# Kernel optimization log

Hardware: AMD Instinct MI355X
Metric: run time of the kernel (lower is better)

## Reference

```python
import jax, jax.numpy as jnp
import numpy as np

# ---- column/activation layout (matches transformer_info init kwarg) ----
N_COLS = 20          # continuous data columns
MODES = 50           # VGM modes per column (gumbel-softmax width)
SPAN = MODES + 1     # 1 tanh scalar + MODES gumbel logits
IN_DIM = 2048
OUT_DIM = N_COLS * SPAN  # 1020
TAU = 0.2
B = 16384
EPS = 1e-9

_spans = []
for i in range(N_COLS):
    st = i * SPAN
    _spans.append((st, st + 1, 0))          # tanh span (alpha)
    _spans.append((st + 1, st + SPAN, 1))   # gumbel-softmax span (beta/d)
N_SEG = len(_spans)

_seg = np.zeros(OUT_DIM, np.int32)   # segment id per output feature
_typ = np.zeros(OUT_DIM, np.int32)   # 0 = tanh, 1 = gumbel-softmax
for si, (s, e, t) in enumerate(_spans):
    _seg[s:e] = si
    _typ[s:e] = t
SEG = jnp.asarray(_seg)
TYP = jnp.asarray(_typ)


def setup_inputs() -> dict:
    key = jax.random.key(0)
    kx, kw, kb, ku = jax.random.split(key, 4)
    bound = 1.0 / np.sqrt(IN_DIM)  # init_bounded(dim=input_dim)
    x = jax.random.normal(kx, (B, IN_DIM), dtype=jnp.float32)
    W = jax.random.uniform(kw, (IN_DIM, OUT_DIM), minval=-bound, maxval=bound, dtype=jnp.float32)
    b = jax.random.uniform(kb, (OUT_DIM,), minval=-bound, maxval=bound, dtype=jnp.float32)
    u = jax.random.uniform(ku, (B, OUT_DIM), dtype=jnp.float32)  # uniform driving gumbel noise
    return {"x": x, "W": W, "b": b, "u": u}


def _segment_softmax(z):
    # softmax over each transformer_info span, fused via segment ops.
    zT = z.T  # [D, B]
    m = jax.ops.segment_max(zT, SEG, num_segments=N_SEG)      # [S, B]
    e = jnp.exp(zT - m[SEG])
    s = jax.ops.segment_sum(e, SEG, num_segments=N_SEG)       # [S, B]
    return (e / s[SEG]).T  # [B, D]


def reference(x, W, b, u):
    outputs = x @ W + b  # [B, OUT_DIM]
    # Gumbel(0,1) noise from uniform u
    g = -jnp.log(-jnp.log(jnp.clip(u, EPS, 1.0 - EPS)))
    soft = _segment_softmax((outputs + g) / TAU)
    # type 0 -> tanh, type 1 -> gumbel-softmax (single fused select)
    data_t = jnp.where(TYP == 0, jnp.tanh(outputs), soft)
    return outputs, data_t
```

## Files before the change

kernel.cpp:

```cpp
#include <hip/hip_runtime.h>
#include <stdint.h>

#define MDIM 16384
#define NDIM 1020
#define KDIM 2048
#define NPAD 1024

typedef __attribute__((ext_vector_type(4))) float f32x4;
typedef __attribute__((ext_vector_type(8))) short short8;

__device__ __forceinline__ unsigned short f2bf(float f) {
    unsigned int u = __float_as_uint(f);
    unsigned int r = (u + 0x7FFFu + ((u >> 16) & 1u)) >> 16;
    return (unsigned short)r;
}

__global__ void prep_w_kernel(const float* __restrict__ W,
                              unsigned short* __restrict__ Wt) {
    const int id = blockIdx.x * 256 + threadIdx.x;
    const int n0 = (id & 255) * 4;
    const int k0 = (id >> 8) * 4;
    float a[4][4];
    if (n0 < NDIM) {
#pragma unroll
        for (int i = 0; i < 4; ++i) {
            const float* p = W + (size_t)(k0 + i) * NDIM + n0;
            a[i][0] = p[0]; a[i][1] = p[1]; a[i][2] = p[2]; a[i][3] = p[3];
        }
    } else {
#pragma unroll
        for (int i = 0; i < 4; ++i)
#pragma unroll
            for (int j = 0; j < 4; ++j) a[i][j] = 0.f;
    }
#pragma unroll
    for (int j = 0; j < 4; ++j) {
        uint2 p;
        p.x = (unsigned)f2bf(a[0][j]) | ((unsigned)f2bf(a[1][j]) << 16);
        p.y = (unsigned)f2bf(a[2][j]) | ((unsigned)f2bf(a[3][j]) << 16);
        *(uint2*)(Wt + (size_t)(n0 + j) * KDIM + k0) = p;
    }
}

__global__ void prep_x_kernel(const float* __restrict__ x,
                              unsigned short* __restrict__ Xb) {
    const size_t total = (size_t)MDIM * KDIM;
    const size_t stride = (size_t)gridDim.x * 256 * 8;
    for (size_t i = ((size_t)blockIdx.x * 256 + threadIdx.x) * 8; i < total; i += stride) {
        const float4 v0 = *(const float4*)(x + i);
        const float4 v1 = *(const float4*)(x + i + 4);
        uint4 p;
        p.x = (unsigned)f2bf(v0.x) | ((unsigned)f2bf(v0.y) << 16);
        p.y = (unsigned)f2bf(v0.z) | ((unsigned)f2bf(v0.w) << 16);
        p.z = (unsigned)f2bf(v1.x) | ((unsigned)f2bf(v1.y) << 16);
        p.w = (unsigned)f2bf(v1.z) | ((unsigned)f2bf(v1.w) << 16);
        *(uint4*)(Xb + i) = p;
    }
}

__global__ void gemm_bf_kernel(const unsigned short* __restrict__ Xb,
                               const unsigned short* __restrict__ Wt,
                               const float* __restrict__ bias,
                               float* __restrict__ out) {
    __shared__ __align__(16) unsigned short As[128][32];
    __shared__ __align__(16) unsigned short Bs[128][32];

    const int tid  = threadIdx.x;
    const int lane = tid & 63;
    const int wid  = tid >> 6;
    const int wr   = wid >> 1;
    const int wc   = wid & 1;
    const int bn   = blockIdx.x;
    const int bm   = blockIdx.y;

    f32x4 acc[4][4];
#pragma unroll
    for (int i = 0; i < 4; ++i)
#pragma unroll
        for (int j = 0; j < 4; ++j) {
            f32x4 z = {0.f, 0.f, 0.f, 0.f};
            acc[i][j] = z;
        }

    const unsigned short* abase =
        Xb + (size_t)(bm * 128 + wid * 16 + (lane >> 2)) * KDIM + (lane & 3) * 8;
    const unsigned short* bbase =
        Wt + (size_t)(bn * 128 + wid * 16 + (lane >> 2)) * KDIM + (lane & 3) * 8;

    for (int kt = 0; kt < KDIM; kt += 32) {
#pragma unroll
        for (int j = 0; j < 2; ++j) {
            __builtin_amdgcn_global_load_lds(
                (const __attribute__((address_space(1))) unsigned int*)(abase + (size_t)j * 64 * KDIM + kt),
                (__attribute__((address_space(3))) unsigned int*)(&As[j * 64 + wid * 16][0]),
                16, 0, 0);
        }
#pragma unroll
        for (int j = 0; j < 2; ++j) {
            __builtin_amdgcn_global_load_lds(
                (const __attribute__((address_space(1))) unsigned int*)(bbase + (size_t)j * 64 * KDIM + kt),
                (__attribute__((address_space(3))) unsigned int*)(&Bs[j * 64 + wid * 16][0]),
                16, 0, 0);
        }
        __syncthreads();

        short8 af[4], bfr[4];
#pragma unroll
        for (int mi = 0; mi < 4; ++mi)
            af[mi] = *(const short8*)&As[wr * 64 + mi * 16 + (lane & 15)][(lane >> 4) * 8];
#pragma unroll
        for (int ni = 0; ni < 4; ++ni)
            bfr[ni] = *(const short8*)&Bs[wc * 64 + ni * 16 + (lane & 15)][(lane >> 4) * 8];

#pragma unroll
        for (int mi = 0; mi < 4; ++mi)
#pragma unroll
            for (int ni = 0; ni < 4; ++ni)
                acc[mi][ni] = __builtin_amdgcn_mfma_f32_16x16x32_bf16(
                    af[mi], bfr[ni], acc[mi][ni], 0, 0, 0);

        __syncthreads();
    }

#pragma unroll
    for (int ni = 0; ni < 4; ++ni) {
        const int col = bn * 128 + wc * 64 + ni * 16 + (lane & 15);
        if (col < NDIM) {
            const float bv = bias[col];
#pragma unroll
            for (int mi = 0; mi < 4; ++mi) {
                const int row = bm * 128 + wr * 64 + mi * 16 + ((lane >> 4) << 2);
                float* op = out + (size_t)row * NDIM + col;
#pragma unroll
                for (int r = 0; r < 4; ++r)
                    op[(size_t)r * NDIM] = acc[mi][ni][r] + bv;
            }
        }
    }
}

__global__ void gemm_kernel(const float* __restrict__ x,
                            const unsigned short* __restrict__ Wt,
                            const float* __restrict__ bias,
                            float* __restrict__ out) {
    __shared__ __align__(16) unsigned short As[128][32];
    __shared__ __align__(16) unsigned short Bs[128][32];

    const int tid  = threadIdx.x;
    const int lane = tid & 63;
    const int wid  = tid >> 6;
    const int wr   = wid >> 1;
    const int wc   = wid & 1;
    const int bn   = blockIdx.x;
    const int bm   = blockIdx.y;

    f32x4 acc[4][4];
#pragma unroll
    for (int i = 0; i < 4; ++i)
#pragma unroll
        for (int j = 0; j < 4; ++j) {
            f32x4 z = {0.f, 0.f, 0.f, 0.f};
            acc[i][j] = z;
        }

    const int arow = tid >> 3;
    const int akg  = tid & 7;
    const float* xbase = x + (size_t)(bm * 128) * KDIM + akg * 4;
    const unsigned short* wbase =
        Wt + (size_t)(bn * 128 + wid * 32 + (lane >> 2)) * KDIM + (lane & 3) * 8;

    for (int kt = 0; kt < KDIM; kt += 32) {
#pragma unroll
        for (int i = 0; i < 4; ++i) {
            const float4 v = *(const float4*)(xbase + (size_t)(i * 32 + arow) * KDIM + kt);
            uint2 p;
            p.x = (unsigned)f2bf(v.x) | ((unsigned)f2bf(v.y) << 16);
            p.y = (unsigned)f2bf(v.z) | ((unsigned)f2bf(v.w) << 16);
            *(uint2*)&As[i * 32 + arow][akg * 4] = p;
        }
#pragma unroll
        for (int j = 0; j < 2; ++j) {
            const unsigned short* src = wbase + (size_t)j * 16 * KDIM + kt;
            __builtin_amdgcn_global_load_lds(
                (const __attribute__((address_space(1))) unsigned int*)src,
                (__attribute__((address_space(3))) unsigned int*)(&Bs[wid * 32 + j * 16][0]),
                16, 0, 0);
        }
        __syncthreads();

        short8 af[4], bfr[4];
#pragma unroll
        for (int mi = 0; mi < 4; ++mi)
            af[mi] = *(const short8*)&As[wr * 64 + mi * 16 + (lane & 15)][(lane >> 4) * 8];
#pragma unroll
        for (int ni = 0; ni < 4; ++ni)
            bfr[ni] = *(const short8*)&Bs[wc * 64 + ni * 16 + (lane & 15)][(lane >> 4) * 8];

#pragma unroll
        for (int mi = 0; mi < 4; ++mi)
#pragma unroll
            for (int ni = 0; ni < 4; ++ni)
                acc[mi][ni] = __builtin_amdgcn_mfma_f32_16x16x32_bf16(
                    af[mi], bfr[ni], acc[mi][ni], 0, 0, 0);

        __syncthreads();
    }

#pragma unroll
    for (int ni = 0; ni < 4; ++ni) {
        const int col = bn * 128 + wc * 64 + ni * 16 + (lane & 15);
        if (col < NDIM) {
            const float bv = bias[col];
#pragma unroll
            for (int mi = 0; mi < 4; ++mi) {
                const int row = bm * 128 + wr * 64 + mi * 16 + ((lane >> 4) << 2);
                float* op = out + (size_t)row * NDIM + col;
#pragma unroll
                for (int r = 0; r < 4; ++r)
                    op[(size_t)r * NDIM] = acc[mi][ni][r] + bv;
            }
        }
    }
}

__global__ void act_kernel(const float* __restrict__ outp,
                           const float* __restrict__ u,
                           float* __restrict__ dt) {
    const int lane  = threadIdx.x & 63;
    const int gwave = (blockIdx.x * 256 + threadIdx.x) >> 6;
    const int nwave = gridDim.x * 4;
    const int total = MDIM * 20;
    const float NEG_INF = -__builtin_inff();

    for (int unit = gwave; unit < total; unit += nwave) {
        const int row = unit / 20;
        const int sp  = unit - row * 20;
        const size_t base = (size_t)row * NDIM + sp * 51;

        float o = 0.f, uu = 0.5f;
        if (lane < 51) {
            o  = outp[base + lane];
            uu = u[base + lane];
        }
        const bool soft = (lane >= 1) && (lane < 51);

        const float uc = fmaxf(uu, 1e-9f);
        const float g  = -__logf(-__logf(uc));
        float z = soft ? (o + g) * 5.0f : NEG_INF;

        float m = z;
#pragma unroll
        for (int off = 32; off; off >>= 1) m = fmaxf(m, __shfl_xor(m, off));
        float e = soft ? __expf(z - m) : 0.f;
        float s = e;
#pragma unroll
        for (int off = 32; off; off >>= 1) s += __shfl_xor(s, off);

        float res;
        if (lane == 0) {
            const float ex = __expf(-2.0f * fabsf(o));
            const float t  = (1.0f - ex) / (1.0f + ex);
            res = copysignf(t, o);
        } else {
            res = e / s;
        }
        if (lane < 51) dt[base + lane] = res;
    }
}

extern "C" void kernel_launch(void* const* d_in, const int* in_sizes, int n_in,
                              void* d_out, int out_size, void* d_ws, size_t ws_size,
                              hipStream_t stream) {
    const float* x = (const float*)d_in[0];
    const float* W = (const float*)d_in[1];
    const float* b = (const float*)d_in[2];
    const float* u = (const float*)d_in[3];
    float* out = (float*)d_out;
    float* dt  = out + (size_t)MDIM * NDIM;
    unsigned short* Wt = (unsigned short*)d_ws;

    prep_w_kernel<<<512, 256, 0, stream>>>(W, Wt);

    const size_t need = ((size_t)NPAD * KDIM + (size_t)MDIM * KDIM) * sizeof(unsigned short);
    if (ws_size >= need) {
        unsigned short* Xb = Wt + (size_t)NPAD * KDIM;
        prep_x_kernel<<<2048, 256, 0, stream>>>(x, Xb);
        gemm_bf_kernel<<<dim3(8, 128), 256, 0, stream>>>(Xb, Wt, b, out);
    } else {
        gemm_kernel<<<dim3(8, 128), 256, 0, stream>>>(x, Wt, b, out);
    }

    act_kernel<<<8192, 256, 0, stream>>>(out, u, dt);
}
```

Before: 212.3 us.

## Add 256x256-tile double-buffered bf16 GEMM with swizzled LDS and staged prefetch

Adds a new GEMM kernel using 256x256 output tiles, 8 waves and 128KB of dynamic LDS. It double-buffers K-steps of 64, interleaving global_load_lds prefetches with MFMA phases under explicit vmcnt waits, barriers and setprio. It also applies an XOR swizzle to LDS columns to avoid bank conflicts and remaps block ids for L2 locality. The larger tiles cut global traffic and sync overhead per FLOP, but 256 blocks on the GPU is coarse-grained, LDS use is very high, and the ws-size guard and fp32 fallback path are removed.

```diff
diff --git a/kernel.cpp b/kernel.cpp
--- a/kernel.cpp
+++ b/kernel.cpp
@@ -5,9 +5,12 @@
 #define NDIM 1020
 #define KDIM 2048
 #define NPAD 1024
+#define TK   (KDIM / 64)
 
 typedef __attribute__((ext_vector_type(4))) float f32x4;
 typedef __attribute__((ext_vector_type(8))) short short8;
+
+#define MFMA16(a, b, c) __builtin_amdgcn_mfma_f32_16x16x32_bf16((a), (b), (c), 0, 0, 0)
 
 __device__ __forceinline__ unsigned short f2bf(float f) {
     unsigned int u = __float_as_uint(f);
@@ -58,6 +61,183 @@
     }
 }
 
+extern "C" __global__ __launch_bounds__(512, 2) void gemm8_kernel(
+    const unsigned short* __restrict__ Xb,
+    const unsigned short* __restrict__ Wt,
+    const float* __restrict__ bias,
+    float* __restrict__ out) {
+    extern __shared__ unsigned short lds_raw[];
+
+    const int tid  = threadIdx.x;
+    const int lane = tid & 63;
+    const int wid  = tid >> 6;
+    const int wr   = wid >> 2;
+    const int wc   = wid & 3;
+
+    const int bid = blockIdx.x;
+    const int swz = (bid & 7) * 32 + (bid >> 3);
+    const int bm  = swz >> 2;
+    const int bn  = swz & 3;
+
+    const int srow = wid * 8 + (lane >> 3);
+    const int scb  = ((lane & 7) ^ (lane >> 3)) * 8;
+    const unsigned short* aS = Xb + (size_t)(bm * 256 + srow) * KDIM + scb;
+    const unsigned short* bS = Wt + (size_t)(bn * 256 + srow) * KDIM + scb;
+
+#define LDS_A(B) (lds_raw + (B) * 32768)
+#define LDS_B(B) (lds_raw + (B) * 32768 + 16384)
+
+#define STAGE(BUFI, OP, STRIPE, S) do {                                          \
+    const size_t ks_ = (size_t)(((S) * 64) & (KDIM - 1));                        \
+    const unsigned short* sp_ =                                                  \
+        ((OP) ? bS : aS) + (size_t)((STRIPE) * 64) * KDIM + ks_;                 \
+    __builtin_amdgcn_global_load_lds(                                            \
+        (const __attribute__((address_space(1))) unsigned int*)sp_,              \
+        (__attribute__((address_space(3))) unsigned int*)(lds_raw +              \
+            (BUFI) * 32768 + (OP) * 16384 + ((STRIPE) * 64 + wid * 8) * 64),     \
+        16, 0, 0);                                                               \
+} while (0)
+
+#define LOAD_AF(DST, BUFI, MF) do {                                              \
+    _Pragma("unroll")                                                            \
+    for (int k2_ = 0; k2_ < 2; ++k2_) {                                          \
+        const int cb_ = ((k2_ * 4 + (lane >> 4)) ^ (lane & 7)) * 8;              \
+        DST[k2_] = *(const short8*)(LDS_A(BUFI) +                                \
+            (wr * 128 + (MF) * 16 + (lane & 15)) * 64 + cb_);                    \
+    }                                                                            \
+} while (0)
+
+#define VMCNT4 do {                                                              \
+    asm volatile("s_waitcnt vmcnt(4)" ::: "memory");                             \
+    __builtin_amdgcn_sched_barrier(0);                                           \
+} while (0)
+
+    f32x4 acc[8][4];
+#pragma unroll
+    for (int i = 0; i < 8; ++i)
+#pragma unroll
+        for (int j = 0; j < 4; ++j) {
+            f32x4 z = {0.f, 0.f, 0.f, 0.f};
+            acc[i][j] = z;
+        }
+
+    STAGE(0, 0, 0, 0); STAGE(0, 0, 1, 0); STAGE(0, 0, 2, 0); STAGE(0, 0, 3, 0);
+    STAGE(0, 1, 0, 0); STAGE(0, 1, 1, 0); STAGE(0, 1, 2, 0); STAGE(0, 1, 3, 0);
+    STAGE(1, 1, 0, 1); STAGE(1, 1, 1, 1); STAGE(1, 1, 2, 1); STAGE(1, 1, 3, 1);
+    STAGE(1, 0, 0, 1); STAGE(1, 0, 2, 1);
+    VMCNT4;
+    __builtin_amdgcn_s_barrier();
+
+    for (int t = 0; t < TK; ++t) {
+        const int buf = t & 1;
+        const int nb  = buf ^ 1;
+        short8 bfv[4][2];
+
+        {
+#pragma unroll
+            for (int nf = 0; nf < 4; ++nf)
+#pragma unroll
+                for (int k2 = 0; k2 < 2; ++k2) {
+                    const int cb = ((k2 * 4 + (lane >> 4)) ^ (lane & 7)) * 8;
+                    bfv[nf][k2] = *(const short8*)(LDS_B(buf) +
+                        (wc * 64 + nf * 16 + (lane & 15)) * 64 + cb);
+                }
+            short8 af0[2], af1[2];
+            LOAD_AF(af0, buf, 0);
+            LOAD_AF(af1, buf, 1);
+            STAGE(nb, 0, 1, t + 1);
+            STAGE(nb, 0, 3, t + 1);
+            __builtin_amdgcn_s_barrier();
+            __builtin_amdgcn_s_setprio(1);
+#pragma unroll
+            for (int nf = 0; nf < 4; ++nf) {
+                acc[0][nf] = MFMA16(af0[0], bfv[nf][0], acc[0][nf]);
+                acc[0][nf] = MFMA16(af0[1], bfv[nf][1], acc[0][nf]);
+                acc[1][nf] = MFMA16(af1[0], bfv[nf][0], acc[1][nf]);
+                acc[1][nf] = MFMA16(af1[1], bfv[nf][1], acc[1][nf]);
+            }
+            __builtin_amdgcn_s_setprio(0);
+            __builtin_amdgcn_s_barrier();
+        }
+        {
+            short8 af0[2], af1[2];
+            LOAD_AF(af0, buf, 2);
+            LOAD_AF(af1, buf, 3);
+            STAGE(buf, 1, 0, t + 2);
+            STAGE(buf, 1, 1, t + 2);
+            __builtin_amdgcn_s_barrier();
+            __builtin_amdgcn_s_setprio(1);
+#pragma unroll
+            for (int nf = 0; nf < 4; ++nf) {
+                acc[2][nf] = MFMA16(af0[0], bfv[nf][0], acc[2][nf]);
+                acc[2][nf] = MFMA16(af0[1], bfv[nf][1], acc[2][nf]);
+                acc[3][nf] = MFMA16(af1[0], bfv[nf][0], acc[3][nf]);
+                acc[3][nf] = MFMA16(af1[1], bfv[nf][1], acc[3][nf]);
+            }
+            __builtin_amdgcn_s_setprio(0);
+            __builtin_amdgcn_s_barrier();
+        }
+        {
+            short8 af0[2], af1[2];
+            LOAD_AF(af0, buf, 4);
+            LOAD_AF(af1, buf, 5);
+            STAGE(buf, 1, 2, t + 2);
+            STAGE(buf, 1, 3, t + 2);
+            __builtin_amdgcn_s_barrier();
+            __builtin_amdgcn_s_setprio(1);
+#pragma unroll
+            for (int nf = 0; nf < 4; ++nf) {
+                acc[4][nf] = MFMA16(af0[0], bfv[nf][0], acc[4][nf]);
+                acc[4][nf] = MFMA16(af0[1], bfv[nf][1], acc[4][nf]);
+                acc[5][nf] = MFMA16(af1[0], bfv[nf][0], acc[5][nf]);
+                acc[5][nf] = MFMA16(af1[1], bfv[nf][1], acc[5][nf]);
+            }
+            __builtin_amdgcn_s_setprio(0);
+            __builtin_amdgcn_s_barrier();
+        }
+        {
+            short8 af0[2], af1[2];
+            LOAD_AF(af0, buf, 6);
+            LOAD_AF(af1, buf, 7);
+            STAGE(buf, 0, 0, t + 2);
+            STAGE(buf, 0, 2, t + 2);
+            __builtin_amdgcn_s_barrier();
+            __builtin_amdgcn_s_setprio(1);
+#pragma unroll
+            for (int nf = 0; nf < 4; ++nf) {
+                acc[6][nf] = MFMA16(af0[0], bfv[nf][0], acc[6][nf]);
+                acc[6][nf] = MFMA16(af0[1], bfv[nf][1], acc[6][nf]);
+                acc[7][nf] = MFMA16(af1[0], bfv[nf][0], acc[7][nf]);
+                acc[7][nf] = MFMA16(af1[1], bfv[nf][1], acc[7][nf]);
+            }
+            __builtin_amdgcn_s_setprio(0);
+            VMCNT4;
+            __builtin_amdgcn_s_barrier();
+        }
+    }
+
+#pragma unroll
+    for (int nf = 0; nf < 4; ++nf) {
+        const int col = bn * 256 + wc * 64 + nf * 16 + (lane & 15);
+        if (col < NDIM) {
+            const float bv = bias[col];
+#pragma unroll
+            for (int mf = 0; mf < 8; ++mf) {
+                const int row = bm * 256 + wr * 128 + mf * 16 + ((lane >> 4) << 2);
+                float* op = out + (size_t)row * NDIM + col;
+#pragma unroll
+                for (int r = 0; r < 4; ++r)
+                    op[(size_t)r * NDIM] = acc[mf][nf][r] + bv;
+            }
+        }
+    }
+#undef LDS_A
+#undef LDS_B
+#undef STAGE
+#undef LOAD_AF
+#undef VMCNT4
+}
+
 __global__ void gemm_bf_kernel(const unsigned short* __restrict__ Xb,
                                const unsigned short* __restrict__ Wt,
                                const float* __restrict__ bias,
@@ -89,19 +269,17 @@
 
     for (int kt = 0; kt < KDIM; kt += 32) {
 #pragma unroll
-        for (int j = 0; j < 2; ++j) {
+        for (int j = 0; j < 2; ++j)
             __builtin_amdgcn_global_load_lds(
                 (const __attribute__((address_space(1))) unsigned int*)(abase + (size_t)j * 64 * KDIM + kt),
                 (__attribute__((address_space(3))) unsigned int*)(&As[j * 64 + wid * 16][0]),
                 16, 0, 0);
-        }
-#pragma unroll
-        for (int j = 0; j < 2; ++j) {
+#pragma unroll
+        for (int j = 0; j < 2; ++j)
             __builtin_amdgcn_global_load_lds(
                 (const __attribute__((address_space(1))) unsigned int*)(bbase + (size_t)j * 64 * KDIM + kt),
                 (__attribute__((address_space(3))) unsigned int*)(&Bs[j * 64 + wid * 16][0]),
                 16, 0, 0);
-        }
         __syncthreads();
 
         short8 af[4], bfr[4];
@@ -116,92 +294,7 @@
         for (int mi = 0; mi < 4; ++mi)
 #pragma unroll
             for (int ni = 0; ni < 4; ++ni)
-                acc[mi][ni] = __builtin_amdgcn_mfma_f32_16x16x32_bf16(
-                    af[mi], bfr[ni], acc[mi][ni], 0, 0, 0);
-
-        __syncthreads();
-    }
-
-#pragma unroll
-    for (int ni = 0; ni < 4; ++ni) {
-        const int col = bn * 128 + wc * 64 + ni * 16 + (lane & 15);
-        if (col < NDIM) {
-            const float bv = bias[col];
-#pragma unroll
-            for (int mi = 0; mi < 4; ++mi) {
-                const int row = bm * 128 + wr * 64 + mi * 16 + ((lane >> 4) << 2);
-                float* op = out + (size_t)row * NDIM + col;
-#pragma unroll
-                for (int r = 0; r < 4; ++r)
-                    op[(size_t)r * NDIM] = acc[mi][ni][r] + bv;
-            }
-        }
-    }
-}
-
-__global__ void gemm_kernel(const float* __restrict__ x,
-                            const unsigned short* __restrict__ Wt,
-                            const float* __restrict__ bias,
-                            float* __restrict__ out) {
-    __shared__ __align__(16) unsigned short As[128][32];
-    __shared__ __align__(16) unsigned short Bs[128][32];
-
-    const int tid  = threadIdx.x;
-    const int lane = tid & 63;
-    const int wid  = tid >> 6;
-    const int wr   = wid >> 1;
-    const int wc   = wid & 1;
-    const int bn   = blockIdx.x;
-    const int bm   = blockIdx.y;
-
-    f32x4 acc[4][4];
-#pragma unroll
-    for (int i = 0; i < 4; ++i)
-#pragma unroll
-        for (int j = 0; j < 4; ++j) {
-            f32x4 z = {0.f, 0.f, 0.f, 0.f};
-            acc[i][j] = z;
-        }
-
-    const int arow = tid >> 3;
-    const int akg  = tid & 7;
-    const float* xbase = x + (size_t)(bm * 128) * KDIM + akg * 4;
-    const unsigned short* wbase =
-        Wt + (size_t)(bn * 128 + wid * 32 + (lane >> 2)) * KDIM + (lane & 3) * 8;
-
-    for (int kt = 0; kt < KDIM; kt += 32) {
-#pragma unroll
-        for (int i = 0; i < 4; ++i) {
-            const float4 v = *(const float4*)(xbase + (size_t)(i * 32 + arow) * KDIM + kt);
-            uint2 p;
-            p.x = (unsigned)f2bf(v.x) | ((unsigned)f2bf(v.y) << 16);
-            p.y = (unsigned)f2bf(v.z) | ((unsigned)f2bf(v.w) << 16);
-            *(uint2*)&As[i * 32 + arow][akg * 4] = p;
-        }
-#pragma unroll
-        for (int j = 0; j < 2; ++j) {
-            const unsigned short* src = wbase + (size_t)j * 16 * KDIM + kt;
-            __builtin_amdgcn_global_load_lds(
-                (const __attribute__((address_space(1))) unsigned int*)src,
-                (__attribute__((address_space(3))) unsigned int*)(&Bs[wid * 32 + j * 16][0]),
-                16, 0, 0);
-        }
-        __syncthreads();
-
-        short8 af[4], bfr[4];
-#pragma unroll
-        for (int mi = 0; mi < 4; ++mi)
-            af[mi] = *(const short8*)&As[wr * 64 + mi * 16 + (lane & 15)][(lane >> 4) * 8];
-#pragma unroll
-        for (int ni = 0; ni < 4; ++ni)
-            bfr[ni] = *(const short8*)&Bs[wc * 64 + ni * 16 + (lane & 15)][(lane >> 4) * 8];
-
-#pragma unroll
-        for (int mi = 0; mi < 4; ++mi)
-#pragma unroll
-            for (int ni = 0; ni < 4; ++ni)
-                acc[mi][ni] = __builtin_amdgcn_mfma_f32_16x16x32_bf16(
-                    af[mi], bfr[ni], acc[mi][ni], 0, 0, 0);
+                acc[mi][ni] = MFMA16(af[mi], bfr[ni], acc[mi][ni]);
 
         __syncthreads();
     }
@@ -278,16 +371,17 @@
     float* out = (float*)d_out;
     float* dt  = out + (size_t)MDIM * NDIM;
     unsigned short* Wt = (unsigned short*)d_ws;
+    unsigned short* Xb = Wt + (size_t)NPAD * KDIM;
 
     prep_w_kernel<<<512, 256, 0, stream>>>(W, Wt);
-
-    const size_t need = ((size_t)NPAD * KDIM + (size_t)MDIM * KDIM) * sizeof(unsigned short);
-    if (ws_size >= need) {
-        unsigned short* Xb = Wt + (size_t)NPAD * KDIM;
-        prep_x_kernel<<<2048, 256, 0, stream>>>(x, Xb);
+    prep_x_kernel<<<2048, 256, 0, stream>>>(x, Xb);
+
+    const hipError_t attr_ok = hipFuncSetAttribute(
+        (const void*)gemm8_kernel, hipFuncAttributeMaxDynamicSharedMemorySize, 131072);
+    if (attr_ok == hipSuccess) {
+        gemm8_kernel<<<256, 512, 131072, stream>>>(Xb, Wt, b, out);
+    } else {
         gemm_bf_kernel<<<dim3(8, 128), 256, 0, stream>>>(Xb, Wt, b, out);
-    } else {
-        gemm_kernel<<<dim3(8, 128), 256, 0, stream>>>(x, Wt, b, out);
     }
 
     act_kernel<<<8192, 256, 0, stream>>>(out, u, dt);
```

Measured after the change: 192.4 us. 9.4% less time.
